# Performance work log

Hardware: AMD Instinct MI355X
Metric: run time of the kernel (lower is better)

Reference implementation:

```python
import jax, jax.numpy as jnp
import numpy as np

B, S, DIM = 2, 2048, 4096
H, KV, HD = 32, 8, 128
REP = H // KV
SCALE = HD ** -0.5
ROPE_THETA = 10000.0


def setup_inputs() -> dict:
    key = jax.random.key(0)
    ks = jax.random.split(key, 6)
    x = jax.random.normal(ks[0], (B, S, DIM), dtype=jnp.float32)
    # weights stored [in, out]; y = x @ W matches nn.Linear(in,out,bias=False)
    wq = jax.random.normal(ks[1], (DIM, H * HD), dtype=jnp.float32) * (DIM ** -0.5)
    wk = jax.random.normal(ks[2], (DIM, KV * HD), dtype=jnp.float32) * (DIM ** -0.5)
    wv = jax.random.normal(ks[3], (DIM, KV * HD), dtype=jnp.float32) * (DIM ** -0.5)
    wo = jax.random.normal(ks[4], (H * HD, DIM), dtype=jnp.float32) * ((H * HD) ** -0.5)
    # RoPE tables: angle[t, j] = t * theta^(-2j/hd)
    inv_freq = 1.0 / (ROPE_THETA ** (np.arange(0, HD, 2, dtype=np.float32) / HD))
    t = np.arange(S, dtype=np.float32)
    angles = np.outer(t, inv_freq)  # [S, HD/2]
    freqs_cos = jnp.asarray(np.cos(angles), dtype=jnp.float32)
    freqs_sin = jnp.asarray(np.sin(angles), dtype=jnp.float32)
    # causal additive mask
    neg = jnp.finfo(jnp.float32).min
    mask = jnp.where(jnp.tril(jnp.ones((S, S), dtype=bool)), 0.0, neg).astype(jnp.float32)
    positions = jnp.arange(S, dtype=jnp.int64)
    return {"x": x, "wq": wq, "wk": wk, "wv": wv, "wo": wo,
            "freqs_cos": freqs_cos, "freqs_sin": freqs_sin,
            "mask": mask, "positions": positions}


def _rope(t, cos, sin):
    # t: [b, s, h, hd]; cos/sin: [s, hd/2]
    b, s, h, hd = t.shape
    tr = t.reshape(b, s, h, hd // 2, 2)
    tre, tim = tr[..., 0], tr[..., 1]
    c = cos[None, :, None, :]
    sn = sin[None, :, None, :]
    out_re = tre * c - tim * sn
    out_im = tre * sn + tim * c
    return jnp.stack([out_re, out_im], axis=-1).reshape(b, s, h, hd)


def reference(x, wq, wk, wv, wo, freqs_cos, freqs_sin, mask, positions):
    b, s, _ = x.shape
    xq = (x @ wq).reshape(b, s, H, HD)
    xk = (x @ wk).reshape(b, s, KV, HD)
    xv = (x @ wv).reshape(b, s, KV, HD)
    xq = _rope(xq, freqs_cos, freqs_sin)
    xk = _rope(xk, freqs_cos, freqs_sin)
    # GQA without materializing repeated KV: group query heads by kv head
    q = xq.transpose(0, 2, 1, 3).reshape(b, KV, REP, s, HD)  # [b,g,r,s,d]
    k = xk.transpose(0, 2, 1, 3)                              # [b,g,s,d]
    v = xv.transpose(0, 2, 1, 3)                              # [b,g,s,d]
    scores = jnp.einsum('bgrqd,bgkd->bgrqk', q, k) * SCALE
    scores = scores + mask[None, None, None, :, :]
    probs = jax.nn.softmax(scores.astype(jnp.float32), axis=-1).astype(q.dtype)
    out = jnp.einsum('bgrqk,bgkd->bgrqd', probs, v)           # [b,g,r,s,d]
    out = out.reshape(b, H, s, HD).transpose(0, 2, 1, 3).reshape(b, s, H * HD)
    return out @ wo
```

## Files before the change

kernel.cpp:

```cpp
#include <hip/hip_runtime.h>
#include <math.h>

#define B_ 2
#define S_ 2048
#define DIM_ 4096
#define H_ 32
#define KV_ 8
#define HD_ 128
#define SCALE_ 0.08838834764831844f
#define QSCALE_ 0.12751744154254998f
#define KVOFF_ 4194304

typedef unsigned short u16;
typedef __attribute__((ext_vector_type(8))) short bf16x8;
typedef __attribute__((ext_vector_type(4))) float f32x4;
typedef __attribute__((ext_vector_type(8))) unsigned short u16x8;
typedef __attribute__((ext_vector_type(4))) unsigned short u16x4;

__device__ __forceinline__ u16 f2b(float f) {
  union { float f; unsigned u; } v; v.f = f;
  unsigned r = v.u + 0x7fffu + ((v.u >> 16) & 1u);
  return (u16)(r >> 16);
}
__device__ __forceinline__ float b2f(u16 h) {
  union { unsigned u; float f; } v; v.u = ((unsigned)h) << 16;
  return v.f;
}
__device__ __forceinline__ unsigned cvt_pk_bf16(float lo, float hi) {
  unsigned r;
  asm("v_cvt_pk_bf16_f32 %0, %1, %2" : "=v"(r) : "v"(lo), "v"(hi));
  return r;
}
__device__ __forceinline__ void async_copy16(const void* g, void* l) {
  __builtin_amdgcn_global_load_lds(
      (const __attribute__((address_space(1))) void*)g,
      (__attribute__((address_space(3))) void*)l, 16, 0, 0);
}
__device__ __forceinline__ void bar() {
  asm volatile("s_barrier" ::: "memory");
}

__global__ __launch_bounds__(256) void cvt_bf16(const float* __restrict__ in,
                                                u16* __restrict__ out, int n4) {
  int i = blockIdx.x * 256 + threadIdx.x;
  if (i >= n4) return;
  float4 v = ((const float4*)in)[i];
  u16x4 o; o[0] = f2b(v.x); o[1] = f2b(v.y); o[2] = f2b(v.z); o[3] = f2b(v.w);
  ((u16x4*)out)[i] = o;
}

__global__ __launch_bounds__(256) void transpose_cvt(
    const float* __restrict__ W, u16* __restrict__ WT, int K, int N) {
  __shared__ float Ts[64][65];
  const int tid = threadIdx.x;
  const int n0 = blockIdx.x * 64, k0 = blockIdx.y * 64;
#pragma unroll
  for (int p = 0; p < 4; ++p) {
    int r = p * 16 + (tid >> 4), c = (tid & 15) * 4;
    float4 v = *(const float4*)(W + (size_t)(k0 + r) * N + n0 + c);
    Ts[r][c] = v.x; Ts[r][c + 1] = v.y; Ts[r][c + 2] = v.z; Ts[r][c + 3] = v.w;
  }
  __syncthreads();
#pragma unroll
  for (int p = 0; p < 4; ++p) {
    int n = p * 16 + (tid >> 4), kq = (tid & 15) * 4;
    u16x4 o;
    o[0] = f2b(Ts[kq + 0][n]); o[1] = f2b(Ts[kq + 1][n]);
    o[2] = f2b(Ts[kq + 2][n]); o[3] = f2b(Ts[kq + 3][n]);
    *(u16x4*)(WT + (size_t)(n0 + n) * K + k0 + kq) = o;
  }
}

__global__ __launch_bounds__(256) void transpose_v(const u16* __restrict__ V,
                                                   u16* __restrict__ Vt) {
  __shared__ u16 Ts[64][72];
  const int tid = threadIdx.x;
  const int s0 = blockIdx.x * 64, d0 = blockIdx.y * 64, hb = blockIdx.z;
  const u16* src = V + ((size_t)hb * S_ + s0) * HD_ + d0;
#pragma unroll
  for (int p = 0; p < 2; ++p) {
    int r = p * 32 + (tid >> 3), seg = (tid & 7) * 8;
    u16x8 v = *(const u16x8*)(src + (size_t)r * HD_ + seg);
#pragma unroll
    for (int j = 0; j < 8; ++j) Ts[r][seg + j] = v[j];
  }
  __syncthreads();
  u16* dst = Vt + ((size_t)hb * HD_ + d0) * S_ + s0;
#pragma unroll
  for (int p = 0; p < 2; ++p) {
    int d = p * 32 + (tid >> 3), seg = (tid & 7) * 8;
    u16x8 o;
#pragma unroll
    for (int j = 0; j < 8; ++j) o[j] = Ts[seg + j][d];
    *(u16x8*)(dst + (size_t)d * S_ + seg) = o;
  }
}

__global__ __launch_bounds__(256) void rope_bf16(unsigned* __restrict__ T,
                                                 const float* __restrict__ cs,
                                                 const float* __restrict__ sn,
                                                 int total, float scale) {
  int idx = blockIdx.x * 256 + threadIdx.x;
  if (idx >= total) return;
  int i = idx & 63, s = (idx >> 6) & (S_ - 1);
  float c = cs[s * 64 + i], si = sn[s * 64 + i];
  unsigned v = T[idx];
  float re = b2f((u16)(v & 0xffffu)), im = b2f((u16)(v >> 16));
  float ore = (re * c - im * si) * scale, oim = (re * si + im * c) * scale;
  T[idx] = (unsigned)f2b(ore) | ((unsigned)f2b(oim) << 16);
}

template <int OUT_MODE>
__global__ __launch_bounds__(256) void gemm_bf16(
    const u16* __restrict__ A, const u16* __restrict__ Bt,
    void* __restrict__ Cout, int M, int N, int K, int heads) {
  __shared__ u16 As[128 * 64];
  __shared__ u16 Bs[128 * 64];
  const int tid = threadIdx.x, lane = tid & 63;
  const int wbase = tid & ~63;
  const int row0 = blockIdx.y * 128, col0 = blockIdx.x * 128;
  const int wm = ((tid >> 6) >> 1) * 64, wn = ((tid >> 6) & 1) * 64;

  f32x4 acc[4][4];
#pragma unroll
  for (int i = 0; i < 4; ++i)
#pragma unroll
    for (int j = 0; j < 4; ++j) acc[i][j] = (f32x4){0.f, 0.f, 0.f, 0.f};

  const int nk = K >> 6;
  for (int kt = 0; kt < nk; ++kt) {
    const int k0 = kt << 6;
#pragma unroll
    for (int i = 0; i < 4; ++i) {
      int g = i * 256 + tid;
      int r = g >> 3, ss = (g & 7) ^ (r & 7);
      async_copy16(A + (size_t)(row0 + r) * K + k0 + ss * 8,
                   (char*)As + (i * 256 + wbase) * 16);
    }
#pragma unroll
    for (int i = 0; i < 4; ++i) {
      int g = i * 256 + tid;
      int r = g >> 3, ss = (g & 7) ^ (r & 7);
      async_copy16(Bt + (size_t)(col0 + r) * K + k0 + ss * 8,
                   (char*)Bs + (i * 256 + wbase) * 16);
    }
    __syncthreads();
#pragma unroll
    for (int ks = 0; ks < 2; ++ks) {
      bf16x8 af[4], bf[4];
#pragma unroll
      for (int mi = 0; mi < 4; ++mi) {
        int r = wm + mi * 16 + (lane & 15);
        int off = (ks * 64 + ((lane >> 4) << 4)) ^ ((r & 7) << 4);
        af[mi] = *(const bf16x8*)((const char*)As + r * 128 + off);
      }
#pragma unroll
      for (int ni = 0; ni < 4; ++ni) {
        int r = wn + ni * 16 + (lane & 15);
        int off = (ks * 64 + ((lane >> 4) << 4)) ^ ((r & 7) << 4);
        bf[ni] = *(const bf16x8*)((const char*)Bs + r * 128 + off);
      }
#pragma unroll
      for (int mi = 0; mi < 4; ++mi)
#pragma unroll
        for (int ni = 0; ni < 4; ++ni)
          acc[mi][ni] = __builtin_amdgcn_mfma_f32_16x16x32_bf16(
              af[mi], bf[ni], acc[mi][ni], 0, 0, 0);
    }
    __syncthreads();
  }

#pragma unroll
  for (int mi = 0; mi < 4; ++mi)
#pragma unroll
    for (int ni = 0; ni < 4; ++ni) {
      int mb = row0 + wm + mi * 16 + ((lane >> 4) << 2);
      int n = col0 + wn + ni * 16 + (lane & 15);
#pragma unroll
      for (int r = 0; r < 4; ++r) {
        int m = mb + r;
        float v = acc[mi][ni][r];
        if (OUT_MODE == 0) {
          ((float*)Cout)[(size_t)m * N + n] = v;
        } else if (OUT_MODE == 1) {
          int b = m >> 11, s = m & (S_ - 1);
          int h = n >> 7, d = n & (HD_ - 1);
          ((u16*)Cout)[(((size_t)(b * heads + h)) * S_ + s) * HD_ + d] = f2b(v);
        } else {
          int b = m >> 11, s = m & (S_ - 1);
          int hh = n >> 7, d = n & (HD_ - 1);
          size_t base = (size_t)(hh >> 3) * KVOFF_;
          ((u16*)Cout)[base + (((size_t)(b * 8 + (hh & 7))) * S_ + s) * HD_ + d] =
              f2b(v);
        }
      }
    }
}

template <int OUT_MODE>
__global__ __launch_bounds__(512) void gemm256(
    const u16* __restrict__ A, const u16* __restrict__ Bt,
    void* __restrict__ Cout, int M, int N, int K, int heads) {
  __shared__ u16 lds[65536];
  char* const ldsb = (char*)lds;
  const int tid = threadIdx.x, lane = tid & 63, wid = tid >> 6;
  const int q = lane & 15, g = lane >> 4;
  const int wm = wid >> 2, wn = wid & 3;
  const int row0 = blockIdx.y * 256, col0 = blockIdx.x * 256;
  const int nk = K >> 6, nh = nk << 2;

  const u16* srcA[2];
  const u16* srcB[2];
#pragma unroll
  for (int u = 0; u < 2; ++u) {
    int j = u * 512 + tid;
    int row = ((j >> 3) << 1) + ((j >> 2) & 1);
    int colg = (j & 3) ^ ((j >> 3) & 3);
    srcA[u] = A + (size_t)(row0 + row) * K + colg * 8;
    srcB[u] = Bt + (size_t)(col0 + row) * K + colg * 8;
  }

  auto STAGE = [&](int h) {
    if (h >= nh) return;
    int tau = h >> 2, ks = (h >> 1) & 1, op = h & 1;
    int slot = (2 * tau + ks) & 3;
    int koff = tau * 64 + ks * 32;
    char* lbase = ldsb + op * 65536 + slot * 16384 + wid * 1024;
#pragma unroll
    for (int u = 0; u < 2; ++u)
      async_copy16((op ? srcB[u] : srcA[u]) + koff, lbase + u * 8192);
  };

  int aread[8], bread[4];
#pragma unroll
  for (int mi = 0; mi < 8; ++mi) {
    int row = wm * 128 + mi * 16 + q;
    aread[mi] = (row >> 1) * 128 + (row & 1) * 64 + ((g ^ ((row >> 1) & 3)) << 4);
  }
#pragma unroll
  for (int ni = 0; ni < 4; ++ni) {
    int row = wn * 64 + ni * 16 + q;
    bread[ni] = (row >> 1) * 128 + (row & 1) * 64 + ((g ^ ((row >> 1) & 3)) << 4);
  }

  f32x4 acc[8][4];
#pragma unroll
  for (int i = 0; i < 8; ++i)
#pragma unroll
    for (int j = 0; j < 4; ++j) acc[i][j] = (f32x4){0.f, 0.f, 0.f, 0.f};

#pragma unroll
  for (int h = 0; h < 6; ++h) STAGE(h);
  asm volatile("s_waitcnt vmcnt(4)" ::: "memory");
  bar();

  for (int t = 0; t < nk; ++t) {
    const int s0 = (2 * t) & 3, s1 = (2 * t + 1) & 3;
    const char* As0 = ldsb + s0 * 16384;
    const char* Bs0 = ldsb + 65536 + s0 * 16384;
    const char* As1 = ldsb + s1 * 16384;
    const char* Bs1 = ldsb + 65536 + s1 * 16384;
    bf16x8 af[4], bfr[4];

#pragma unroll
    for (int i = 0; i < 4; ++i) af[i] = *(const bf16x8*)(As0 + aread[i]);
#pragma unroll
    for (int i = 0; i < 4; ++i) bfr[i] = *(const bf16x8*)(Bs0 + bread[i]);
    STAGE(4 * t + 6);
    bar();
    __builtin_amdgcn_s_setprio(1);
#pragma unroll
    for (int mi = 0; mi < 4; ++mi)
#pragma unroll
      for (int ni = 0; ni < 4; ++ni)
        acc[mi][ni] = __builtin_amdgcn_mfma_f32_16x16x32_bf16(
            af[mi], bfr[ni], acc[mi][ni], 0, 0, 0);
    __builtin_amdgcn_s_setprio(0);
    bar();

#pragma unroll
    for (int i = 0; i < 4; ++i) af[i] = *(const bf16x8*)(As0 + aread[4 + i]);
    STAGE(4 * t + 7);
    bar();
    __builtin_amdgcn_s_setprio(1);
#pragma unroll
    for (int mi = 0; mi < 4; ++mi)
#pragma unroll
      for (int ni = 0; ni < 4; ++ni)
        acc[4 + mi][ni] = __builtin_amdgcn_mfma_f32_16x16x32_bf16(
            af[mi], bfr[ni], acc[4 + mi][ni], 0, 0, 0);
    __builtin_amdgcn_s_setprio(0);
    bar();

#pragma unroll
    for (int i = 0; i < 4; ++i) af[i] = *(const bf16x8*)(As1 + aread[i]);
#pragma unroll
    for (int i = 0; i < 4; ++i) bfr[i] = *(const bf16x8*)(Bs1 + bread[i]);
    STAGE(4 * t + 8);
    bar();
    __builtin_amdgcn_s_setprio(1);
#pragma unroll
    for (int mi = 0; mi < 4; ++mi)
#pragma unroll
      for (int ni = 0; ni < 4; ++ni)
        acc[mi][ni] = __builtin_amdgcn_mfma_f32_16x16x32_bf16(
            af[mi], bfr[ni], acc[mi][ni], 0, 0, 0);
    __builtin_amdgcn_s_setprio(0);
    bar();

#pragma unroll
    for (int i = 0; i < 4; ++i) af[i] = *(const bf16x8*)(As1 + aread[4 + i]);
    STAGE(4 * t + 9);
    bar();
    __builtin_amdgcn_s_setprio(1);
#pragma unroll
    for (int mi = 0; mi < 4; ++mi)
#pragma unroll
      for (int ni = 0; ni < 4; ++ni)
        acc[4 + mi][ni] = __builtin_amdgcn_mfma_f32_16x16x32_bf16(
            af[mi], bfr[ni], acc[4 + mi][ni], 0, 0, 0);
    __builtin_amdgcn_s_setprio(0);
    if (t < nk - 2)
      asm volatile("s_waitcnt vmcnt(4)" ::: "memory");
    else if (t == nk - 2)
      asm volatile("s_waitcnt vmcnt(0)" ::: "memory");
    bar();
  }

#pragma unroll
  for (int mi = 0; mi < 8; ++mi)
#pragma unroll
    for (int ni = 0; ni < 4; ++ni) {
      int mb = row0 + wm * 128 + mi * 16 + (g << 2);
      int n = col0 + wn * 64 + ni * 16 + q;
#pragma unroll
      for (int r = 0; r < 4; ++r) {
        int m = mb + r;
        float v = acc[mi][ni][r];
        if (OUT_MODE == 0) {
          ((float*)Cout)[(size_t)m * N + n] = v;
        } else {
          int b = m >> 11, s = m & (S_ - 1);
          int h = n >> 7, d = n & (HD_ - 1);
          ((u16*)Cout)[(((size_t)(b * heads + h)) * S_ + s) * HD_ + d] = f2b(v);
        }
      }
    }
}

__global__ __launch_bounds__(256) void attn_mfma(
    const u16* __restrict__ Qb, const u16* __restrict__ Kb,
    const u16* __restrict__ Vt, u16* __restrict__ AO,
    const float* __restrict__ fc, const float* __restrict__ fs) {
  __shared__ u16 Ks[64 * 128];
  __shared__ u16 Vs[128 * 64];
  __shared__ u16 Ps[4][16 * 64];

  const int tid = threadIdx.x, lane = tid & 63, wid = tid >> 6;
  const int wbase = tid & ~63;
  const int pid = blockIdx.x, h = blockIdx.y, b = blockIdx.z;
  const int kvh = h >> 2;
  const int qq = lane & 15, g = lane >> 4;

  const u16* Kbase = Kb + ((size_t)(b * KV_ + kvh) * S_) * HD_;
  const u16* Vbase = Vt + ((size_t)(b * KV_ + kvh) * HD_) * S_;

  const u16* Kl[4];
  const u16* Vl[4];
#pragma unroll
  for (int i = 0; i < 4; ++i) {
    int gg = i * 256 + tid;
    int rK = gg >> 4, ssK = (gg & 15) ^ (rK & 7);
    Kl[i] = Kbase + (size_t)rK * HD_ + ssK * 8;
    int rV = gg >> 3, ssV = (gg & 7) ^ (rV & 7);
    Vl[i] = Vbase + (size_t)rV * S_ + ssV * 8;
  }
  char* const pw = (char*)Ps[wid];

  for (int half = 0; half < 2; ++half) {
    const int qt = half ? (31 - pid) : pid;
    const int q0 = qt * 64;

    bf16x8 qf[4];
    {
      const int srow = q0 + wid * 16 + qq;
      const u16* qrow = Qb + ((size_t)(b * H_ + h) * S_ + srow) * HD_ + (g << 3);
      const float* cb = fc + srow * 64 + (g << 2);
      const float* sb = fs + srow * 64 + (g << 2);
#pragma unroll
      for (int ks = 0; ks < 4; ++ks) {
        u16x8 v = *(const u16x8*)(qrow + ks * 32);
        float4 cv = *(const float4*)(cb + ks * 16);
        float4 sv = *(const float4*)(sb + ks * 16);
        unsigned w[4];
#pragma unroll
        for (int j = 0; j < 4; ++j) {
          float c = ((const float*)&cv)[j] * QSCALE_;
          float s = ((const float*)&sv)[j] * QSCALE_;
          float re = b2f((u16)v[2 * j]), im = b2f((u16)v[2 * j + 1]);
          w[j] = cvt_pk_bf16(re * c - im * s, re * s + im * c);
        }
        union { unsigned u[4]; bf16x8 q; } cvt;
        cvt.u[0] = w[0]; cvt.u[1] = w[1]; cvt.u[2] = w[2]; cvt.u[3] = w[3];
        qf[ks] = cvt.q;
      }
    }

    f32x4 oacc[8];
#pragma unroll
    for (int i = 0; i < 8; ++i) oacc[i] = (f32x4){0.f, 0.f, 0.f, 0.f};
    float mrow = -3e38f, lrow = 0.f;

    for (int kt = 0; kt <= qt; ++kt) {
      const int kv0 = kt * 64;
#pragma unroll
      for (int i = 0; i < 4; ++i)
        async_copy16(Kl[i] + (size_t)kv0 * HD_, (char*)Ks + (i * 256 + wbase) * 16);
#pragma unroll
      for (int i = 0; i < 4; ++i)
        async_copy16(Vl[i] + kv0, (char*)Vs + (i * 256 + wbase) * 16);
      __syncthreads();

      f32x4 sacc[4];
#pragma unroll
      for (int nf = 0; nf < 4; ++nf) sacc[nf] = (f32x4){0.f, 0.f, 0.f, 0.f};
#pragma unroll
      for (int nf = 0; nf < 4; ++nf) {
        int r = nf * 16 + qq;
        const char* base = (const char*)Ks + r * 256;
#pragma unroll
        for (int ks = 0; ks < 4; ++ks) {
          int off = (ks * 64 + (g << 4)) ^ ((r & 7) << 4);
          bf16x8 kf = *(const bf16x8*)(base + off);
          sacc[nf] =
              __builtin_amdgcn_mfma_f32_16x16x32_bf16(kf, qf[ks], sacc[nf], 0, 0, 0);
        }
      }

      float rmax = -3e38f;
      if (kt == qt) {
        const int qg = q0 + wid * 16 + qq;
#pragma unroll
        for (int nf = 0; nf < 4; ++nf)
#pragma unroll
          for (int r = 0; r < 4; ++r) {
            int kg = kv0 + nf * 16 + g * 4 + r;
            float sv = (kg > qg) ? -3e38f : sacc[nf][r];
            sacc[nf][r] = sv;
            rmax = fmaxf(rmax, sv);
          }
      } else {
#pragma unroll
        for (int nf = 0; nf < 4; ++nf)
#pragma unroll
          for (int r = 0; r < 4; ++r) rmax = fmaxf(rmax, sacc[nf][r]);
      }
      rmax = fmaxf(rmax, __shfl_xor(rmax, 16, 64));
      rmax = fmaxf(rmax, __shfl_xor(rmax, 32, 64));
      const bool defer = __all(rmax - mrow <= 11.5f);
      float mnew, fsc;
      if (defer) {
        mnew = mrow; fsc = 1.0f;
      } else {
        mnew = fmaxf(mrow, rmax); fsc = exp2f(mrow - mnew);
      }
      mrow = mnew;
      float psum = 0.f;
#pragma unroll
      for (int nf = 0; nf < 4; ++nf)
#pragma unroll
        for (int r = 0; r < 4; ++r) {
          float p = exp2f(sacc[nf][r] - mnew);
          sacc[nf][r] = p;
          psum += p;
        }
      psum += __shfl_xor(psum, 16, 64);
      psum += __shfl_xor(psum, 32, 64);
      lrow = lrow * fsc + psum;

      if (!defer) {
        const float fr0 = __shfl(fsc, g * 4 + 0);
        const float fr1 = __shfl(fsc, g * 4 + 1);
        const float fr2 = __shfl(fsc, g * 4 + 2);
        const float fr3 = __shfl(fsc, g * 4 + 3);
#pragma unroll
        for (int df = 0; df < 8; ++df) {
          oacc[df][0] *= fr0; oacc[df][1] *= fr1;
          oacc[df][2] *= fr2; oacc[df][3] *= fr3;
        }
      }

#pragma unroll
      for (int nf = 0; nf < 4; ++nf) {
        uint2 pk;
        pk.x = cvt_pk_bf16(sacc[nf][0], sacc[nf][1]);
        pk.y = cvt_pk_bf16(sacc[nf][2], sacc[nf][3]);
        int gran = (nf * 2 + (g >> 1)) ^ (qq & 7);
        *(uint2*)(pw + qq * 128 + gran * 16 + (g & 1) * 8) = pk;
      }

#pragma unroll
      for (int ks = 0; ks < 2; ++ks) {
        int poff = qq * 128 + ((ks * 64 + (g << 4)) ^ ((qq & 7) << 4));
        bf16x8 pf = *(const bf16x8*)(pw + poff);
#pragma unroll
        for (int df = 0; df < 8; ++df) {
          int vr = df * 16 + qq;
          int voff = (ks * 64 + (g << 4)) ^ ((vr & 7) << 4);
          bf16x8 vf = *(const bf16x8*)((const char*)Vs + vr * 128 + voff);
          oacc[df] =
              __builtin_amdgcn_mfma_f32_16x16x32_bf16(pf, vf, oacc[df], 0, 0, 0);
        }
      }
      __syncthreads();
    }

    const float linv = 1.f / lrow;
    const float i0 = __shfl(linv, g * 4 + 0);
    const float i1 = __shfl(linv, g * 4 + 1);
    const float i2 = __shfl(linv, g * 4 + 2);
    const float i3 = __shfl(linv, g * 4 + 3);
    const float inv[4] = {i0, i1, i2, i3};
#pragma unroll
    for (int df = 0; df < 8; ++df)
#pragma unroll
      for (int r = 0; r < 4; ++r) {
        int sq = q0 + wid * 16 + g * 4 + r;
        AO[(size_t)(b * S_ + sq) * (H_ * HD_) + h * HD_ + df * 16 + qq] =
            f2b(oacc[df][r] * inv[r]);
      }
  }
}

extern "C" void kernel_launch(void* const* d_in, const int* in_sizes, int n_in,
                              void* d_out, int out_size, void* d_ws, size_t ws_size,
                              hipStream_t stream) {
  const float* x  = (const float*)d_in[0];
  const float* wq = (const float*)d_in[1];
  const float* wk = (const float*)d_in[2];
  const float* wv = (const float*)d_in[3];
  const float* wo = (const float*)d_in[4];
  const float* fc = (const float*)d_in[5];
  const float* fs = (const float*)d_in[6];
  float* out = (float*)d_out;

  u16* ws  = (u16*)d_ws;
  u16* wqT = ws;
  u16* VtB = ws;
  u16* xb  = ws + 16777216;
  u16* AOb = xb;
  u16* woT = ws + 33554432;
  u16* Qh  = ws + 50331648;
  u16* wkT = ws + 67108864;
  u16* wvT = ws + 71303168;
  u16* Kh  = ws + 75497472;
  u16* Vh  = ws + 79691776;

  dim3 blk(256);

  cvt_bf16<<<dim3(16384), blk, 0, stream>>>(x, xb, 4194304);
  transpose_cvt<<<dim3(64, 64), blk, 0, stream>>>(wq, wqT, DIM_, H_ * HD_);
  transpose_cvt<<<dim3(16, 64), blk, 0, stream>>>(wk, wkT, DIM_, KV_ * HD_);
  transpose_cvt<<<dim3(16, 64), blk, 0, stream>>>(wv, wvT, DIM_, KV_ * HD_);
  transpose_cvt<<<dim3(64, 64), blk, 0, stream>>>(wo, woT, H_ * HD_, DIM_);

  gemm256<1><<<dim3(16, 16), dim3(512), 0, stream>>>(xb, wqT, Qh, 4096, 4096, 4096, H_);
  gemm_bf16<2><<<dim3(16, 32), blk, 0, stream>>>(xb, wkT, Kh, 4096, 2048, 4096, KV_);

  rope_bf16<<<dim3(8192), blk, 0, stream>>>((unsigned*)Kh, fc, fs, 2097152, 1.0f);

  transpose_v<<<dim3(32, 2, 16), blk, 0, stream>>>(Vh, VtB);

  attn_mfma<<<dim3(16, 32, 2), blk, 0, stream>>>(Qh, Kh, VtB, AOb, fc, fs);

  gemm256<0><<<dim3(16, 16), dim3(512), 0, stream>>>(AOb, woT, out, 4096, 4096, 4096, 0);
}
```

Before: 557.4 us.

## Switch attention to 32x32x16 MFMA with 128-row query tiles and register-resident P

```diff
diff --git a/kernel.cpp b/kernel.cpp
--- a/kernel.cpp
+++ b/kernel.cpp
@@ -14,6 +14,7 @@
 typedef unsigned short u16;
 typedef __attribute__((ext_vector_type(8))) short bf16x8;
 typedef __attribute__((ext_vector_type(4))) float f32x4;
+typedef __attribute__((ext_vector_type(16))) float f32x16;
 typedef __attribute__((ext_vector_type(8))) unsigned short u16x8;
 typedef __attribute__((ext_vector_type(4))) unsigned short u16x4;
 
@@ -348,19 +349,18 @@
     }
 }
 
-__global__ __launch_bounds__(256) void attn_mfma(
+__global__ __launch_bounds__(256, 2) void attn_mfma(
     const u16* __restrict__ Qb, const u16* __restrict__ Kb,
     const u16* __restrict__ Vt, u16* __restrict__ AO,
     const float* __restrict__ fc, const float* __restrict__ fs) {
   __shared__ u16 Ks[64 * 128];
   __shared__ u16 Vs[128 * 64];
-  __shared__ u16 Ps[4][16 * 64];
 
   const int tid = threadIdx.x, lane = tid & 63, wid = tid >> 6;
   const int wbase = tid & ~63;
   const int pid = blockIdx.x, h = blockIdx.y, b = blockIdx.z;
   const int kvh = h >> 2;
-  const int qq = lane & 15, g = lane >> 4;
+  const int l31 = lane & 31, hi = lane >> 5;
 
   const u16* Kbase = Kb + ((size_t)(b * KV_ + kvh) * S_) * HD_;
   const u16* Vbase = Vt + ((size_t)(b * KV_ + kvh) * HD_) * S_;
@@ -375,23 +375,22 @@
     int rV = gg >> 3, ssV = (gg & 7) ^ (rV & 7);
     Vl[i] = Vbase + (size_t)rV * S_ + ssV * 8;
   }
-  char* const pw = (char*)Ps[wid];
 
   for (int half = 0; half < 2; ++half) {
-    const int qt = half ? (31 - pid) : pid;
-    const int q0 = qt * 64;
-
-    bf16x8 qf[4];
+    const int qt = half ? (15 - pid) : pid;
+    const int q0 = qt * 128;
+    const int qg = q0 + wid * 32 + l31;
+
+    bf16x8 qf[8];
     {
-      const int srow = q0 + wid * 16 + qq;
-      const u16* qrow = Qb + ((size_t)(b * H_ + h) * S_ + srow) * HD_ + (g << 3);
-      const float* cb = fc + srow * 64 + (g << 2);
-      const float* sb = fs + srow * 64 + (g << 2);
-#pragma unroll
-      for (int ks = 0; ks < 4; ++ks) {
-        u16x8 v = *(const u16x8*)(qrow + ks * 32);
-        float4 cv = *(const float4*)(cb + ks * 16);
-        float4 sv = *(const float4*)(sb + ks * 16);
+      const u16* qrow = Qb + ((size_t)(b * H_ + h) * S_ + qg) * HD_ + hi * 8;
+      const float* cb = fc + qg * 64 + hi * 4;
+      const float* sb = fs + qg * 64 + hi * 4;
+#pragma unroll
+      for (int ks = 0; ks < 8; ++ks) {
+        u16x8 v = *(const u16x8*)(qrow + ks * 16);
+        float4 cv = *(const float4*)(cb + ks * 8);
+        float4 sv = *(const float4*)(sb + ks * 8);
         unsigned w[4];
 #pragma unroll
         for (int j = 0; j < 4; ++j) {
@@ -406,12 +405,15 @@
       }
     }
 
-    f32x4 oacc[8];
-#pragma unroll
-    for (int i = 0; i < 8; ++i) oacc[i] = (f32x4){0.f, 0.f, 0.f, 0.f};
+    f32x16 oacc[4];
+#pragma unroll
+    for (int i = 0; i < 4; ++i)
+#pragma unroll
+      for (int j = 0; j < 16; ++j) oacc[i][j] = 0.f;
     float mrow = -3e38f, lrow = 0.f;
 
-    for (int kt = 0; kt <= qt; ++kt) {
+    const int nkt = 2 * qt + 2;
+    for (int kt = 0; kt < nkt; ++kt) {
       const int kv0 = kt * 64;
 #pragma unroll
       for (int i = 0; i < 4; ++i)
@@ -421,41 +423,38 @@
         async_copy16(Vl[i] + kv0, (char*)Vs + (i * 256 + wbase) * 16);
       __syncthreads();
 
-      f32x4 sacc[4];
-#pragma unroll
-      for (int nf = 0; nf < 4; ++nf) sacc[nf] = (f32x4){0.f, 0.f, 0.f, 0.f};
-#pragma unroll
-      for (int nf = 0; nf < 4; ++nf) {
-        int r = nf * 16 + qq;
-        const char* base = (const char*)Ks + r * 256;
-#pragma unroll
-        for (int ks = 0; ks < 4; ++ks) {
-          int off = (ks * 64 + (g << 4)) ^ ((r & 7) << 4);
-          bf16x8 kf = *(const bf16x8*)(base + off);
-          sacc[nf] =
-              __builtin_amdgcn_mfma_f32_16x16x32_bf16(kf, qf[ks], sacc[nf], 0, 0, 0);
-        }
+      f32x16 sacc[2];
+#pragma unroll
+      for (int kf = 0; kf < 2; ++kf)
+#pragma unroll
+        for (int j = 0; j < 16; ++j) sacc[kf][j] = 0.f;
+#pragma unroll
+      for (int ks = 0; ks < 8; ++ks) {
+#pragma unroll
+        for (int kf = 0; kf < 2; ++kf) {
+          const int arow = kf * 32 + l31;
+          bf16x8 kfrag = *(const bf16x8*)(
+              (const char*)Ks + arow * 256 + ((((ks * 2 + hi) << 4)) ^ ((arow & 7) << 4)));
+          sacc[kf] = __builtin_amdgcn_mfma_f32_32x32x16_bf16(kfrag, qf[ks],
+                                                             sacc[kf], 0, 0, 0);
+        }
+      }
+
+      if (kv0 + 63 > q0 + wid * 32) {
+#pragma unroll
+        for (int kf = 0; kf < 2; ++kf)
+#pragma unroll
+          for (int r = 0; r < 16; ++r) {
+            int kg = kv0 + kf * 32 + (r & 3) + 8 * (r >> 2) + 4 * hi;
+            if (kg > qg) sacc[kf][r] = -3e38f;
+          }
       }
 
       float rmax = -3e38f;
-      if (kt == qt) {
-        const int qg = q0 + wid * 16 + qq;
-#pragma unroll
-        for (int nf = 0; nf < 4; ++nf)
-#pragma unroll
-          for (int r = 0; r < 4; ++r) {
-            int kg = kv0 + nf * 16 + g * 4 + r;
-            float sv = (kg > qg) ? -3e38f : sacc[nf][r];
-            sacc[nf][r] = sv;
-            rmax = fmaxf(rmax, sv);
-          }
-      } else {
-#pragma unroll
-        for (int nf = 0; nf < 4; ++nf)
-#pragma unroll
-          for (int r = 0; r < 4; ++r) rmax = fmaxf(rmax, sacc[nf][r]);
-      }
-      rmax = fmaxf(rmax, __shfl_xor(rmax, 16, 64));
+#pragma unroll
+      for (int kf = 0; kf < 2; ++kf)
+#pragma unroll
+        for (int r = 0; r < 16; ++r) rmax = fmaxf(rmax, sacc[kf][r]);
       rmax = fmaxf(rmax, __shfl_xor(rmax, 32, 64));
       const bool defer = __all(rmax - mrow <= 11.5f);
       float mnew, fsc;
@@ -467,68 +466,71 @@
       mrow = mnew;
       float psum = 0.f;
 #pragma unroll
-      for (int nf = 0; nf < 4; ++nf)
-#pragma unroll
-        for (int r = 0; r < 4; ++r) {
-          float p = exp2f(sacc[nf][r] - mnew);
-          sacc[nf][r] = p;
+      for (int kf = 0; kf < 2; ++kf)
+#pragma unroll
+        for (int r = 0; r < 16; ++r) {
+          float p = exp2f(sacc[kf][r] - mnew);
+          sacc[kf][r] = p;
           psum += p;
         }
-      psum += __shfl_xor(psum, 16, 64);
       psum += __shfl_xor(psum, 32, 64);
       lrow = lrow * fsc + psum;
 
       if (!defer) {
-        const float fr0 = __shfl(fsc, g * 4 + 0);
-        const float fr1 = __shfl(fsc, g * 4 + 1);
-        const float fr2 = __shfl(fsc, g * 4 + 2);
-        const float fr3 = __shfl(fsc, g * 4 + 3);
-#pragma unroll
-        for (int df = 0; df < 8; ++df) {
-          oacc[df][0] *= fr0; oacc[df][1] *= fr1;
-          oacc[df][2] *= fr2; oacc[df][3] *= fr3;
-        }
-      }
-
-#pragma unroll
-      for (int nf = 0; nf < 4; ++nf) {
-        uint2 pk;
-        pk.x = cvt_pk_bf16(sacc[nf][0], sacc[nf][1]);
-        pk.y = cvt_pk_bf16(sacc[nf][2], sacc[nf][3]);
-        int gran = (nf * 2 + (g >> 1)) ^ (qq & 7);
-        *(uint2*)(pw + qq * 128 + gran * 16 + (g & 1) * 8) = pk;
-      }
-
-#pragma unroll
-      for (int ks = 0; ks < 2; ++ks) {
-        int poff = qq * 128 + ((ks * 64 + (g << 4)) ^ ((qq & 7) << 4));
-        bf16x8 pf = *(const bf16x8*)(pw + poff);
-#pragma unroll
-        for (int df = 0; df < 8; ++df) {
-          int vr = df * 16 + qq;
-          int voff = (ks * 64 + (g << 4)) ^ ((vr & 7) << 4);
-          bf16x8 vf = *(const bf16x8*)((const char*)Vs + vr * 128 + voff);
-          oacc[df] =
-              __builtin_amdgcn_mfma_f32_16x16x32_bf16(pf, vf, oacc[df], 0, 0, 0);
+#pragma unroll
+        for (int r = 0; r < 16; ++r) {
+          float fr = __shfl(fsc, (r & 3) + 8 * (r >> 2) + 4 * hi, 64);
+#pragma unroll
+          for (int df = 0; df < 4; ++df) oacc[df][r] *= fr;
+        }
+      }
+
+      bf16x8 pa[4];
+#pragma unroll
+      for (int kf = 0; kf < 2; ++kf) {
+        unsigned w0 = cvt_pk_bf16(sacc[kf][0], sacc[kf][1]);
+        unsigned w1 = cvt_pk_bf16(sacc[kf][2], sacc[kf][3]);
+        unsigned w2 = cvt_pk_bf16(sacc[kf][4], sacc[kf][5]);
+        unsigned w3 = cvt_pk_bf16(sacc[kf][6], sacc[kf][7]);
+        unsigned w4 = cvt_pk_bf16(sacc[kf][8], sacc[kf][9]);
+        unsigned w5 = cvt_pk_bf16(sacc[kf][10], sacc[kf][11]);
+        unsigned w6 = cvt_pk_bf16(sacc[kf][12], sacc[kf][13]);
+        unsigned w7 = cvt_pk_bf16(sacc[kf][14], sacc[kf][15]);
+        asm volatile("v_permlane32_swap_b32 %0, %1" : "+v"(w0), "+v"(w2));
+        asm volatile("v_permlane32_swap_b32 %0, %1" : "+v"(w1), "+v"(w3));
+        asm volatile("v_permlane32_swap_b32 %0, %1" : "+v"(w4), "+v"(w6));
+        asm volatile("v_permlane32_swap_b32 %0, %1" : "+v"(w5), "+v"(w7));
+        union { unsigned u[4]; bf16x8 q; } f0, f1;
+        f0.u[0] = w0; f0.u[1] = w1; f0.u[2] = w2; f0.u[3] = w3;
+        f1.u[0] = w4; f1.u[1] = w5; f1.u[2] = w6; f1.u[3] = w7;
+        pa[kf * 2] = f0.q;
+        pa[kf * 2 + 1] = f1.q;
+      }
+
+#pragma unroll
+      for (int ks = 0; ks < 4; ++ks) {
+#pragma unroll
+        for (int df = 0; df < 4; ++df) {
+          const int vrow = df * 32 + l31;
+          bf16x8 vf = *(const bf16x8*)(
+              (const char*)Vs + vrow * 128 + ((((ks * 2 + hi) << 4)) ^ ((vrow & 7) << 4)));
+          oacc[df] = __builtin_amdgcn_mfma_f32_32x32x16_bf16(pa[ks], vf,
+                                                             oacc[df], 0, 0, 0);
         }
       }
       __syncthreads();
     }
 
     const float linv = 1.f / lrow;
-    const float i0 = __shfl(linv, g * 4 + 0);
-    const float i1 = __shfl(linv, g * 4 + 1);
-    const float i2 = __shfl(linv, g * 4 + 2);
-    const float i3 = __shfl(linv, g * 4 + 3);
-    const float inv[4] = {i0, i1, i2, i3};
-#pragma unroll
-    for (int df = 0; df < 8; ++df)
-#pragma unroll
-      for (int r = 0; r < 4; ++r) {
-        int sq = q0 + wid * 16 + g * 4 + r;
-        AO[(size_t)(b * S_ + sq) * (H_ * HD_) + h * HD_ + df * 16 + qq] =
-            f2b(oacc[df][r] * inv[r]);
-      }
+#pragma unroll
+    for (int r = 0; r < 16; ++r) {
+      const int qloc = (r & 3) + 8 * (r >> 2) + 4 * hi;
+      const float invq = __shfl(linv, qloc, 64);
+      const int sq = q0 + wid * 32 + qloc;
+      u16* dst = AO + (size_t)(b * S_ + sq) * (H_ * HD_) + h * HD_ + l31;
+#pragma unroll
+      for (int df = 0; df < 4; ++df) dst[df * 32] = f2b(oacc[df][r] * invq);
+    }
   }
 }
 
@@ -571,7 +573,7 @@
 
   transpose_v<<<dim3(32, 2, 16), blk, 0, stream>>>(Vh, VtB);
 
-  attn_mfma<<<dim3(16, 32, 2), blk, 0, stream>>>(Qh, Kh, VtB, AOb, fc, fs);
+  attn_mfma<<<dim3(8, 32, 2), blk, 0, stream>>>(Qh, Kh, VtB, AOb, fc, fs);
 
   gemm256<0><<<dim3(16, 16), dim3(512), 0, stream>>>(AOb, woT, out, 4096, 4096, 4096, 0);
 }
```

Result: faster. 515.7 us (-7.5%).
